# Kernel tuning notes

Hardware: AMD Instinct MI355X
Metric: run time of the kernel (lower is better)

Reference implementation:

```python
import jax, jax.numpy as jnp
import numpy as np

N = 50000
E = 800000
F_IN = 96
HID = 128
NCLS = 40
EPS = 0.0  # GINConv default eps


def _mlp(h, W1, b1, W2, b2):
    # Linear -> ReLU -> Linear
    h = jax.nn.relu(h @ W1 + b1)
    return h @ W2 + b2


def _gin_conv(x, edge_index, W1, b1, W2, b2):
    src, dst = edge_index[0], edge_index[1]
    # sum-aggregate neighbor features: scatter-add x[src] into dst
    agg = jax.ops.segment_sum(x[src], dst, num_segments=N)
    return _mlp((1.0 + EPS) * x + agg, W1, b1, W2, b2)


def setup_inputs() -> dict:
    key = jax.random.key(0)
    ks = jax.random.split(key, 12)

    def lin(kw, fan_in, fan_out):
        bound = 1.0 / np.sqrt(fan_in)
        k1, k2 = jax.random.split(kw)
        W = jax.random.uniform(k1, (fan_in, fan_out), jnp.float32, -bound, bound)
        b = jax.random.uniform(k2, (fan_out,), jnp.float32, -bound, bound)
        return W, b

    x = jax.random.normal(ks[0], (N, F_IN), jnp.float32)
    edge_index = jax.random.randint(ks[1], (2, E), 0, N, jnp.int64)
    W1a, b1a = lin(ks[2], F_IN, HID)
    W2a, b2a = lin(ks[3], HID, HID)
    W1b, b1b = lin(ks[4], HID, HID)
    W2b, b2b = lin(ks[5], HID, HID)
    Wfc, bfc = lin(ks[6], HID, NCLS)
    return {"x": x, "edge_index": edge_index,
            "W1a": W1a, "b1a": b1a, "W2a": W2a, "b2a": b2a,
            "W1b": W1b, "b1b": b1b, "W2b": W2b, "b2b": b2b,
            "Wfc": Wfc, "bfc": bfc}


def reference(x, edge_index, W1a, b1a, W2a, b2a, W1b, b1b, W2b, b2b, Wfc, bfc):
    h = _gin_conv(x, edge_index, W1a, b1a, W2a, b2a)
    h = jax.nn.relu(h)
    h = _gin_conv(h, edge_index, W1b, b1b, W2b, b2b)
    return h @ Wfc + bfc  # [N, NCLS]
```

## Files before the change

### kernel.cpp

```cpp
#include <hip/hip_runtime.h>

constexpr int N_NODES = 50000;
constexpr int N_EDGES = 800000;
constexpr int F_INPUT = 96;
constexpr int HID = 128;
constexpr int NCLS = 40;
constexpr int REC = 64;
constexpr int ENT = 62;

typedef __attribute__((ext_vector_type(8))) short short8;
typedef __attribute__((ext_vector_type(4))) float f32x4;

__device__ __forceinline__ float bf2f(unsigned int u16) {
    unsigned int x = u16 << 16;
    return __builtin_bit_cast(float, x);
}
__device__ __forceinline__ unsigned short f2bf(float f) {
    unsigned int x = __builtin_bit_cast(unsigned int, f);
    x += 0x7fffu + ((x >> 16) & 1u);
    return (unsigned short)(x >> 16);
}

constexpr int PB_FILL = N_EDGES / 256;
constexpr int PB_XC = (N_NODES * F_INPUT / 4 + 255) / 256;
constexpr int PB_X0 = PB_FILL;
constexpr int PB_F0 = PB_X0 + PB_XC;
constexpr int PB_W1 = PB_F0 + 33;
constexpr int PB_W2 = PB_W1 + 48;
constexpr int PB_W3 = PB_W2 + 64;
constexpr int PB_END = PB_W3 + 64;

__global__ __launch_bounds__(256) void prep_all(
    const float* __restrict__ x,
    const float* __restrict__ W1a, const float* __restrict__ W2a,
    const float* __restrict__ W1b, const float* __restrict__ W2b,
    const float* __restrict__ b2b, const float* __restrict__ Wfc,
    const float* __restrict__ bfc, const int* __restrict__ ei,
    unsigned short* __restrict__ W1aT, unsigned short* __restrict__ W2aT,
    unsigned short* __restrict__ W1bT, unsigned short* __restrict__ WcT,
    float* __restrict__ bc, unsigned short* __restrict__ bucket,
    unsigned short* __restrict__ xb) {
    const int b = blockIdx.x;
    const int tid = threadIdx.x;
    if (b < PB_FILL) {
        int e = b * 256 + tid;
        int s = ei[e];
        int d = ei[N_EDGES + e];
        int pos = atomicAdd(reinterpret_cast<int*>(&bucket[(size_t)d * REC]), 1);
        if (pos < ENT) bucket[(size_t)d * REC + 2 + pos] = (unsigned short)s;
    } else if (b < PB_F0) {
        int e4 = ((b - PB_X0) * 256 + tid) * 4;
        if (e4 < N_NODES * F_INPUT) {
            float4 v = *reinterpret_cast<const float4*>(&x[e4]);
            uint2 o;
            o.x = (unsigned int)f2bf(v.x) | ((unsigned int)f2bf(v.y) << 16);
            o.y = (unsigned int)f2bf(v.z) | ((unsigned int)f2bf(v.w) << 16);
            *reinterpret_cast<uint2*>(&xb[e4]) = o;
        }
    } else if (b < PB_W1) {
        int idx = (b - PB_F0) * 256 + tid;
        if (idx < 64 * 128) {
            int n = idx >> 7, k = idx & 127;
            float s = 0.f;
            if (n < NCLS) {
                for (int j = 0; j < 128; ++j) s += W2b[k * 128 + j] * Wfc[j * NCLS + n];
            }
            WcT[idx] = f2bf(s);
        } else if (idx < 64 * 128 + 64) {
            int n = idx - 64 * 128;
            float s = 0.f;
            if (n < NCLS) {
                s = bfc[n];
                for (int j = 0; j < 128; ++j) s += b2b[j] * Wfc[j * NCLS + n];
            }
            bc[n] = s;
        }
    } else if (b < PB_W2) {
        int idx = (b - PB_W1) * 256 + tid;
        int n = idx / 96, k = idx % 96;
        W1aT[idx] = f2bf(W1a[k * 128 + n]);
    } else if (b < PB_W3) {
        int idx = (b - PB_W2) * 256 + tid;
        int n = idx >> 7, k = idx & 127;
        W2aT[idx] = f2bf(W2a[k * 128 + n]);
    } else {
        int idx = (b - PB_W3) * 256 + tid;
        int n = idx >> 7, k = idx & 127;
        W1bT[idx] = f2bf(W1b[k * 128 + n]);
    }
}

template<int F>
__global__ __launch_bounds__(256) void gather_bf(const unsigned short* __restrict__ X,
                                                 const unsigned short* __restrict__ bucket,
                                                 unsigned short* __restrict__ OUT) {
    const int wave = threadIdx.x >> 6;
    const int lane = threadIdx.x & 63;
    const int node = blockIdx.x * 4 + wave;
    if (node >= N_NODES) return;
    const unsigned short* rec = &bucket[(size_t)node * REC];
    int deg = *reinterpret_cast<const int*>(rec);
    if (deg > ENT) deg = ENT;

    int v = (lane < deg) ? (int)rec[2 + lane] : 0x7fffffff;
#pragma unroll
    for (int k = 2; k <= 64; k <<= 1) {
#pragma unroll
        for (int j = k >> 1; j > 0; j >>= 1) {
            int pv = __shfl_xor(v, j, 64);
            bool keepmin = (((lane & k) == 0) == ((lane & j) == 0));
            v = keepmin ? (pv < v ? pv : v) : (pv > v ? pv : v);
        }
    }

    const int f = lane * 2;
    const bool act = (f < F);
    float a0 = 0.f, a1 = 0.f;
    int j = 0;
    for (; j + 7 < deg; j += 8) {
        int s[8];
        unsigned int vv[8];
#pragma unroll
        for (int q = 0; q < 8; ++q) s[q] = __shfl(v, j + q, 64);
#pragma unroll
        for (int q = 0; q < 8; ++q) {
            if (act) vv[q] = *reinterpret_cast<const unsigned int*>(&X[(size_t)s[q] * F + f]);
        }
        if (act) {
#pragma unroll
            for (int q = 0; q < 8; ++q) {
                a0 += bf2f(vv[q] & 0xffff);
                a1 += bf2f(vv[q] >> 16);
            }
        }
    }
    if (j + 3 < deg) {
        int s[4];
        unsigned int vv[4];
#pragma unroll
        for (int q = 0; q < 4; ++q) s[q] = __shfl(v, j + q, 64);
#pragma unroll
        for (int q = 0; q < 4; ++q) {
            if (act) vv[q] = *reinterpret_cast<const unsigned int*>(&X[(size_t)s[q] * F + f]);
        }
        if (act) {
#pragma unroll
            for (int q = 0; q < 4; ++q) {
                a0 += bf2f(vv[q] & 0xffff);
                a1 += bf2f(vv[q] >> 16);
            }
        }
        j += 4;
    }
    for (; j < deg; ++j) {
        int s = __shfl(v, j, 64);
        if (act) {
            unsigned int vx = *reinterpret_cast<const unsigned int*>(&X[(size_t)s * F + f]);
            a0 += bf2f(vx & 0xffff);
            a1 += bf2f(vx >> 16);
        }
    }
    if (act) {
        unsigned int xv = *reinterpret_cast<const unsigned int*>(&X[(size_t)node * F + f]);
        a0 += bf2f(xv & 0xffff);
        a1 += bf2f(xv >> 16);
        unsigned int o = (unsigned int)f2bf(a0) | ((unsigned int)f2bf(a1) << 16);
        *reinterpret_cast<unsigned int*>(&OUT[(size_t)node * F + f]) = o;
    }
}

template<int K1, int NT2, int NCOUT, bool RELU2, bool BF16_OUT>
__global__ __launch_bounds__(256) void mlp_fused(const unsigned short* __restrict__ A,
                                                 const unsigned short* __restrict__ W1T,
                                                 const float* __restrict__ b1,
                                                 const unsigned short* __restrict__ W2T,
                                                 const float* __restrict__ b2,
                                                 void* __restrict__ Cout, int M) {
    constexpr int KS1 = K1 / 32;
    constexpr int NT1 = 8;
    constexpr int K2 = 128;
    constexpr int KS2 = K2 / 32;
    __shared__ __align__(16) unsigned short sH[4][16][136];

    const int tid = threadIdx.x;
    const int lane = tid & 63;
    const int wv = tid >> 6;
    const int rowbase = blockIdx.x * 64 + wv * 16;
    const int rA = lane & 15;
    const int kg = lane >> 4;

    int r0 = rowbase + rA;
    if (r0 >= M) r0 = M - 1;
    const unsigned short* ap = A + (size_t)r0 * K1 + kg * 8;
    const unsigned short* b1p = W1T + (size_t)rA * K1 + kg * 8;

    f32x4 acc1[NT1] = {};
#pragma unroll
    for (int ks = 0; ks < KS1; ++ks) {
        short8 a = *reinterpret_cast<const short8*>(ap + ks * 32);
#pragma unroll
        for (int nt = 0; nt < NT1; ++nt) {
            short8 b = *reinterpret_cast<const short8*>(b1p + nt * 16 * K1 + ks * 32);
            acc1[nt] = __builtin_amdgcn_mfma_f32_16x16x32_bf16(a, b, acc1[nt], 0, 0, 0);
        }
    }

    const int oc = lane & 15;
    const int orow = (lane >> 4) * 4;
#pragma unroll
    for (int nt = 0; nt < NT1; ++nt) {
        float bz = b1[nt * 16 + oc];
#pragma unroll
        for (int r = 0; r < 4; ++r) {
            float v = fmaxf(acc1[nt][r] + bz, 0.f);
            sH[wv][orow + r][nt * 16 + oc] = f2bf(v);
        }
    }
    __syncthreads();

    const unsigned short* b2p = W2T + (size_t)rA * K2 + kg * 8;
    f32x4 acc2[NT2] = {};
#pragma unroll
    for (int ks = 0; ks < KS2; ++ks) {
        short8 a = *reinterpret_cast<const short8*>(&sH[wv][rA][kg * 8 + ks * 32]);
#pragma unroll
        for (int nt = 0; nt < NT2; ++nt) {
            short8 b = *reinterpret_cast<const short8*>(b2p + nt * 16 * K2 + ks * 32);
            acc2[nt] = __builtin_amdgcn_mfma_f32_16x16x32_bf16(a, b, acc2[nt], 0, 0, 0);
        }
    }

#pragma unroll
    for (int nt = 0; nt < NT2; ++nt) {
        int col = nt * 16 + oc;
        if (col >= NCOUT) continue;
        float bz = b2[col];
#pragma unroll
        for (int r = 0; r < 4; ++r) {
            int row = rowbase + orow + r;
            if (row < M) {
                float v = acc2[nt][r] + bz;
                if (RELU2) v = fmaxf(v, 0.f);
                if (BF16_OUT)
                    ((unsigned short*)Cout)[(size_t)row * NCOUT + col] = f2bf(v);
                else
                    ((float*)Cout)[(size_t)row * NCOUT + col] = v;
            }
        }
    }
}

extern "C" void kernel_launch(void* const* d_in, const int* in_sizes, int n_in,
                              void* d_out, int out_size, void* d_ws, size_t ws_size,
                              hipStream_t stream) {
    const float* x   = (const float*)d_in[0];
    const int*   ei  = (const int*)d_in[1];
    const float* W1a = (const float*)d_in[2];
    const float* b1a = (const float*)d_in[3];
    const float* W2a = (const float*)d_in[4];
    const float* b2a = (const float*)d_in[5];
    const float* W1b = (const float*)d_in[6];
    const float* b1b = (const float*)d_in[7];
    const float* W2b = (const float*)d_in[8];
    const float* b2b = (const float*)d_in[9];
    const float* Wfc = (const float*)d_in[10];
    const float* bfc = (const float*)d_in[11];
    float* out = (float*)d_out;

    char* p = (char*)d_ws;
    auto alloc = [&](size_t bytes) {
        char* r = p;
        p += (bytes + 255) & ~size_t(255);
        return r;
    };
    unsigned short* xb   = (unsigned short*)alloc((size_t)N_NODES * F_INPUT * 2);
    unsigned short* h0   = (unsigned short*)alloc((size_t)N_NODES * F_INPUT * 2);
    unsigned short* t    = (unsigned short*)alloc((size_t)N_NODES * HID * 2);
    unsigned short* g    = (unsigned short*)alloc((size_t)N_NODES * HID * 2);
    unsigned short* W1aT = (unsigned short*)alloc(128 * 96 * 2);
    unsigned short* W2aT = (unsigned short*)alloc(128 * 128 * 2);
    unsigned short* W1bT = (unsigned short*)alloc(128 * 128 * 2);
    unsigned short* WcT  = (unsigned short*)alloc(64 * 128 * 2);
    float* bc            = (float*)alloc(64 * 4);
    unsigned short* bucket = (unsigned short*)alloc((size_t)N_NODES * REC * 2);

    const int nb4 = (N_NODES + 3) / 4;
    const int mb = (N_NODES + 63) / 64;

    hipMemsetAsync(bucket, 0, (size_t)N_NODES * REC * 2, stream);

    prep_all<<<PB_END, 256, 0, stream>>>(x, W1a, W2a, W1b, W2b, b2b, Wfc, bfc, ei,
                                         W1aT, W2aT, W1bT, WcT, bc, bucket, xb);

    gather_bf<F_INPUT><<<nb4, 256, 0, stream>>>(xb, bucket, h0);
    mlp_fused<96, 8, 128, true, true><<<mb, 256, 0, stream>>>(h0, W1aT, b1a, W2aT, b2a, t,
                                                              N_NODES);

    gather_bf<HID><<<nb4, 256, 0, stream>>>(t, bucket, g);
    mlp_fused<128, 4, 40, false, false><<<mb, 256, 0, stream>>>(g, W1bT, b1b, WcT, bc, out,
                                                                N_NODES);
}
```

Before: 255.9 us.

## Replace global-atomic bucket fill with per-block LDS-counter scan over compacted dst

```diff
diff --git a/kernel.cpp b/kernel.cpp
--- a/kernel.cpp
+++ b/kernel.cpp
@@ -21,14 +21,14 @@
     return (unsigned short)(x >> 16);
 }
 
-constexpr int PB_FILL = N_EDGES / 256;
-constexpr int PB_XC = (N_NODES * F_INPUT / 4 + 255) / 256;
-constexpr int PB_X0 = PB_FILL;
-constexpr int PB_F0 = PB_X0 + PB_XC;
-constexpr int PB_W1 = PB_F0 + 33;
-constexpr int PB_W2 = PB_W1 + 48;
-constexpr int PB_W3 = PB_W2 + 64;
-constexpr int PB_END = PB_W3 + 64;
+constexpr int PA_XC = (N_NODES * F_INPUT / 4 + 255) / 256;
+constexpr int PA_DC = (N_EDGES / 4 + 255) / 256;
+constexpr int PA_D0 = PA_XC;
+constexpr int PA_F0 = PA_D0 + PA_DC;
+constexpr int PA_W1 = PA_F0 + 33;
+constexpr int PA_W2 = PA_W1 + 48;
+constexpr int PA_W3 = PA_W2 + 64;
+constexpr int PA_END = PA_W3 + 64;
 
 __global__ __launch_bounds__(256) void prep_all(
     const float* __restrict__ x,
@@ -38,18 +38,12 @@
     const float* __restrict__ bfc, const int* __restrict__ ei,
     unsigned short* __restrict__ W1aT, unsigned short* __restrict__ W2aT,
     unsigned short* __restrict__ W1bT, unsigned short* __restrict__ WcT,
-    float* __restrict__ bc, unsigned short* __restrict__ bucket,
+    float* __restrict__ bc, unsigned short* __restrict__ dstc,
     unsigned short* __restrict__ xb) {
     const int b = blockIdx.x;
     const int tid = threadIdx.x;
-    if (b < PB_FILL) {
-        int e = b * 256 + tid;
-        int s = ei[e];
-        int d = ei[N_EDGES + e];
-        int pos = atomicAdd(reinterpret_cast<int*>(&bucket[(size_t)d * REC]), 1);
-        if (pos < ENT) bucket[(size_t)d * REC + 2 + pos] = (unsigned short)s;
-    } else if (b < PB_F0) {
-        int e4 = ((b - PB_X0) * 256 + tid) * 4;
+    if (b < PA_D0) {
+        int e4 = (b * 256 + tid) * 4;
         if (e4 < N_NODES * F_INPUT) {
             float4 v = *reinterpret_cast<const float4*>(&x[e4]);
             uint2 o;
@@ -57,8 +51,17 @@
             o.y = (unsigned int)f2bf(v.z) | ((unsigned int)f2bf(v.w) << 16);
             *reinterpret_cast<uint2*>(&xb[e4]) = o;
         }
-    } else if (b < PB_W1) {
-        int idx = (b - PB_F0) * 256 + tid;
+    } else if (b < PA_F0) {
+        int e4 = ((b - PA_D0) * 256 + tid) * 4;
+        if (e4 < N_EDGES) {
+            int4 d = *reinterpret_cast<const int4*>(&ei[N_EDGES + e4]);
+            uint2 o;
+            o.x = (unsigned int)(unsigned short)d.x | ((unsigned int)(unsigned short)d.y << 16);
+            o.y = (unsigned int)(unsigned short)d.z | ((unsigned int)(unsigned short)d.w << 16);
+            *reinterpret_cast<uint2*>(&dstc[e4]) = o;
+        }
+    } else if (b < PA_W1) {
+        int idx = (b - PA_F0) * 256 + tid;
         if (idx < 64 * 128) {
             int n = idx >> 7, k = idx & 127;
             float s = 0.f;
@@ -75,18 +78,49 @@
             }
             bc[n] = s;
         }
-    } else if (b < PB_W2) {
-        int idx = (b - PB_W1) * 256 + tid;
+    } else if (b < PA_W2) {
+        int idx = (b - PA_W1) * 256 + tid;
         int n = idx / 96, k = idx % 96;
         W1aT[idx] = f2bf(W1a[k * 128 + n]);
-    } else if (b < PB_W3) {
-        int idx = (b - PB_W2) * 256 + tid;
+    } else if (b < PA_W3) {
+        int idx = (b - PA_W2) * 256 + tid;
         int n = idx >> 7, k = idx & 127;
         W2aT[idx] = f2bf(W2a[k * 128 + n]);
     } else {
-        int idx = (b - PB_W3) * 256 + tid;
+        int idx = (b - PA_W3) * 256 + tid;
         int n = idx >> 7, k = idx & 127;
         W1bT[idx] = f2bf(W1b[k * 128 + n]);
+    }
+}
+
+__global__ __launch_bounds__(1024) void fill_scan(const int* __restrict__ ei,
+                                                  const unsigned int* __restrict__ dstc2,
+                                                  unsigned short* __restrict__ bucket) {
+    constexpr int NPB = (N_NODES + 255) / 256;
+    __shared__ int lcnt[NPB];
+    const int base = blockIdx.x * NPB;
+    const int nloc = min(NPB, N_NODES - base);
+    for (int i = threadIdx.x; i < NPB; i += 1024) lcnt[i] = 0;
+    __syncthreads();
+    constexpr int NU = N_EDGES / 2;
+    for (int u = threadIdx.x; u < NU; u += 1024) {
+        unsigned int pk = dstc2[u];
+        int e0 = u * 2;
+        int d0 = (int)(pk & 0xffffu), d1 = (int)(pk >> 16);
+        int r0 = d0 - base, r1 = d1 - base;
+        if ((unsigned)r0 < (unsigned)nloc) {
+            int pos = atomicAdd(&lcnt[r0], 1);
+            if (pos < ENT) bucket[(size_t)d0 * REC + 2 + pos] = (unsigned short)ei[e0];
+        }
+        if ((unsigned)r1 < (unsigned)nloc) {
+            int pos = atomicAdd(&lcnt[r1], 1);
+            if (pos < ENT) bucket[(size_t)d1 * REC + 2 + pos] = (unsigned short)ei[e0 + 1];
+        }
+    }
+    __syncthreads();
+    for (int i = threadIdx.x; i < nloc; i += 1024) {
+        int c = lcnt[i];
+        *reinterpret_cast<int*>(&bucket[(size_t)(base + i) * REC]) = (c > ENT ? ENT : c);
     }
 }
 
@@ -282,15 +316,16 @@
     unsigned short* W1bT = (unsigned short*)alloc(128 * 128 * 2);
     unsigned short* WcT  = (unsigned short*)alloc(64 * 128 * 2);
     float* bc            = (float*)alloc(64 * 4);
+    unsigned short* dstc = (unsigned short*)alloc((size_t)N_EDGES * 2);
     unsigned short* bucket = (unsigned short*)alloc((size_t)N_NODES * REC * 2);
 
     const int nb4 = (N_NODES + 3) / 4;
     const int mb = (N_NODES + 63) / 64;
 
-    hipMemsetAsync(bucket, 0, (size_t)N_NODES * REC * 2, stream);
-
-    prep_all<<<PB_END, 256, 0, stream>>>(x, W1a, W2a, W1b, W2b, b2b, Wfc, bfc, ei,
-                                         W1aT, W2aT, W1bT, WcT, bc, bucket, xb);
+    prep_all<<<PA_END, 256, 0, stream>>>(x, W1a, W2a, W1b, W2b, b2b, Wfc, bfc, ei,
+                                         W1aT, W2aT, W1bT, WcT, bc, dstc, xb);
+
+    fill_scan<<<256, 1024, 0, stream>>>(ei, (const unsigned int*)dstc, bucket);
 
     gather_bf<F_INPUT><<<nb4, 256, 0, stream>>>(xb, bucket, h0);
     mlp_fused<96, 8, 128, true, true><<<mb, 256, 0, stream>>>(h0, W1aT, b1a, W2aT, b2a, t,
```

New measurement: 361.3 us. 41.2% more time.
